# Kernel optimization log

Hardware: AMD Instinct MI355X
Metric: run time of the kernel (lower is better)

Reference implementation:

```python
import jax, jax.numpy as jnp
import numpy as np

BLOCK, HALO, HEADS, DH = 8, 4, 4, 32
EPS = 1e-5


def _convT(x, w, p):
    # torch ConvTranspose2d(stride=1, padding=p) == conv with flipped/transposed kernel, padding k-1-p
    k = w.shape[-1]
    w2 = jnp.flip(w, axis=(-2, -1)).transpose(1, 0, 2, 3)  # (Cin,Cout,k,k) -> (Cout,Cin,k,k)
    pad = k - 1 - p
    return jax.lax.conv_general_dilated(x, w2, (1, 1), ((pad, pad), (pad, pad)),
                                        dimension_numbers=('NCHW', 'OIHW', 'NCHW'))


def _bn(x, g, b, m, v):
    s = g * jax.lax.rsqrt(v + EPS)
    return x * s[None, :, None, None] + (b - m * s)[None, :, None, None]


def _rel_to_abs(x):
    # x: [b, l, 2r-1] -> [b, l, r]
    b, l, m = x.shape
    r = (m + 1) // 2
    x = jnp.concatenate([x, jnp.zeros((b, l, 1), x.dtype)], axis=2)
    flat = jnp.concatenate([x.reshape(b, l * (m + 1)), jnp.zeros((b, m - l), x.dtype)], axis=1)
    return flat.reshape(b, l + 1, m)[:, :l, -r:]


def _rel_logits_1d(q, rel_k):
    # q: [b, x, y, d]; rel_k: [2r-1, d] -> [b, x, r, y, r]
    b, x, y, d = q.shape
    r = (rel_k.shape[0] + 1) // 2
    logits = jnp.einsum('bxyd,rd->bxyr', q, rel_k)
    logits = _rel_to_abs(logits.reshape(b * x, y, -1)).reshape(b, x, y, r)
    return jnp.broadcast_to(logits[:, :, None, :, :], (b, x, r, y, r))


def _rel_pos_emb(q, rel_h, rel_w):
    # q: [bb, block*block, dh] (already scaled, per halonet-pytorch)
    bb, n, d = q.shape
    qg = q.reshape(bb, BLOCK, BLOCK, d)
    lw = _rel_logits_1d(qg, rel_w).transpose(0, 1, 3, 2, 4).reshape(bb, n, -1)  # b (x y) (i j)
    lh = _rel_logits_1d(qg.transpose(0, 2, 1, 3), rel_h).transpose(0, 3, 1, 4, 2).reshape(bb, n, -1)  # b (y x) (j i)
    return lw + lh


def _halo_attn(x, to_q, to_kv, to_out_w, to_out_b, rel_h, rel_w):
    B, C, H, W = x.shape
    b, h = BLOCK, HALO
    nh, nw = H // b, W // b
    nblk = nh * nw
    wsz = b + 2 * h
    inner = to_q.shape[1]
    scale = DH ** -0.5
    # queries: non-overlapping blocks -> [B*nblk, b*b, C]
    q_inp = x.reshape(B, C, nh, b, nw, b).transpose(0, 2, 4, 3, 5, 1).reshape(B * nblk, b * b, C)
    # keys/values: overlapping halo windows (F.unfold) -> [B*nblk, wsz*wsz, C]
    pat = jax.lax.conv_general_dilated_patches(x, (wsz, wsz), (b, b), ((h, h), (h, h)))  # [B, C*wsz*wsz, nh, nw]
    kv_inp = pat.reshape(B, C, wsz * wsz, nblk).transpose(0, 3, 2, 1).reshape(B * nblk, wsz * wsz, C)
    q = q_inp @ to_q
    k, v = jnp.split(kv_inp @ to_kv, 2, axis=-1)
    def heads(t):
        return t.reshape(t.shape[0], t.shape[1], HEADS, DH).transpose(0, 2, 1, 3).reshape(-1, t.shape[1], DH)
    q, k, v = heads(q) * scale, heads(k), heads(v)
    sim = jnp.einsum('bid,bjd->bij', q, k) + _rel_pos_emb(q, rel_h, rel_w)  # [B*nblk*HEADS, b*b, wsz*wsz]
    # mask out halo positions that fall into zero padding
    ones = jnp.ones((1, 1, H, W), x.dtype)
    mpat = jax.lax.conv_general_dilated_patches(ones, (wsz, wsz), (b, b), ((h, h), (h, h)))
    mask = mpat.reshape(wsz * wsz, nblk).T > 0  # [nblk, wsz*wsz]
    neg = -jnp.finfo(sim.dtype).max
    sim = jnp.where(mask[None, :, None, None, :],
                    sim.reshape(B, nblk, HEADS, b * b, wsz * wsz), neg)
    attn = jax.nn.softmax(sim, axis=-1).reshape(-1, b * b, wsz * wsz)
    out = jnp.einsum('bij,bjd->bid', attn, v)
    out = out.reshape(B * nblk, HEADS, b * b, DH).transpose(0, 2, 1, 3).reshape(B * nblk, b * b, inner)
    out = out @ to_out_w + to_out_b
    return out.reshape(B, nh, nw, b, b, C).transpose(0, 5, 1, 3, 2, 4).reshape(B, C, H, W)


def setup_inputs() -> dict:
    key = jax.random.key(0)
    ks = jax.random.split(key, 13)
    B, C, H, W = 2, 128, 192, 192
    inner = HEADS * DH
    rel = 2 * (BLOCK + 2 * HALO) - 1  # 31
    n = lambda k, s, sc: jax.random.normal(k, s, jnp.float32) * sc
    return {
        'x': jax.random.normal(ks[0], (B, C, H, W), jnp.float32),
        'conv1_w': n(ks[1], (C, C, 1, 1), 0.1),
        'bn1_g': jnp.ones((C,), jnp.float32), 'bn1_b': jnp.zeros((C,), jnp.float32),
        'bn1_m': n(ks[2], (C,), 0.1),
        'bn1_v': jax.random.uniform(ks[3], (C,), jnp.float32, 0.5, 1.5),
        'to_q': n(ks[4], (C, inner), 0.05), 'to_kv': n(ks[5], (C, 2 * inner), 0.05),
        'to_out_w': n(ks[6], (inner, C), 0.05), 'to_out_b': n(ks[7], (C,), 0.01),
        'rel_h': n(ks[8], (rel, DH), DH ** -0.5), 'rel_w': n(ks[9], (rel, DH), DH ** -0.5),
        'conv3_w': n(ks[10], (C, C, 3, 3), 0.05),
        'bn3_g': jnp.ones((C,), jnp.float32), 'bn3_b': jnp.zeros((C,), jnp.float32),
        'bn3_m': n(ks[11], (C,), 0.1),
        'bn3_v': jax.random.uniform(ks[12], (C,), jnp.float32, 0.5, 1.5),
    }


def reference(x, conv1_w, bn1_g, bn1_b, bn1_m, bn1_v, to_q, to_kv, to_out_w, to_out_b,
              rel_h, rel_w, conv3_w, bn3_g, bn3_b, bn3_m, bn3_v):
    # Bottleneck (stride=1, no downsample): conv1x1T -> BN -> ReLU -> HaloAttention -> ReLU
    #   -> conv3x3T -> BN -> +identity -> ReLU
    out = jax.nn.relu(_bn(_convT(x, conv1_w, 0), bn1_g, bn1_b, bn1_m, bn1_v))
    out = jax.nn.relu(_halo_attn(out, to_q, to_kv, to_out_w, to_out_b, rel_h, rel_w))
    out = _bn(_convT(out, conv3_w, 1), bn3_g, bn3_b, bn3_m, bn3_v)
    return jax.nn.relu(out + x)
```

## Files before the change

### kernel.cpp

```cpp
#include <hip/hip_runtime.h>
#include <hip/hip_bf16.h>

using bf16 = __hip_bfloat16;
typedef unsigned short u16;
typedef unsigned int   u32;
typedef __attribute__((ext_vector_type(8))) short short8;
typedef __attribute__((ext_vector_type(4))) float f32x4;

#define B_N 2
#define CCH 128
#define HH 192
#define WW 192
#define HWS (HH*WW)
#define NBLKS 576
#define EPSV 1e-5f
#define LDW 136

__device__ __forceinline__ float b2f(bf16 v){ return __bfloat162float(v); }
__device__ __forceinline__ bf16  f2b(float v){ return __float2bfloat16(v); }
__device__ __forceinline__ u32 pck(float a, float b){
    bf16 x = f2b(a), y = f2b(b);
    return (u32)*(u16*)&x | ((u32)*(u16*)&y << 16);
}

__global__ __launch_bounds__(256) void prep_w(
    const float* __restrict__ w1, const float* __restrict__ to_q,
    const float* __restrict__ to_kv, const float* __restrict__ to_ow,
    const float* __restrict__ w3, const float* __restrict__ relh,
    const float* __restrict__ relw, bf16* __restrict__ wb)
{
    int i = blockIdx.x*256 + threadIdx.x;
    float v;
    if (i < 16384){       int co=(i>>7)&127, ci=i&127;      v = w1[ci*128+co]; }
    else if (i < 32768){  int r=i-16384; int co=r>>7, ci=r&127; v = to_q[ci*128+co]*0.17677669529663687f; }
    else if (i < 49152){  int r=i-32768; int co=r>>7, ci=r&127; v = to_kv[ci*256+co]; }
    else if (i < 65536){  int r=i-49152; int co=r>>7, ci=r&127; v = to_kv[ci*256+128+co]; }
    else if (i < 81920){  int r=i-65536; int co=r>>7, ci=r&127; v = to_ow[ci*128+co]; }
    else if (i < 229376){ int r=i-81920; int tap=r>>14, co=(r>>7)&127, ci=r&127; int a=tap/3, b=tap-a*3;
                          v = w3[((size_t)(ci*128+co)*3+a)*3+b]; }
    else if (i < 230400){ int j=i-229376; v = (j < 992) ? relh[j] : 0.f; }
    else                { int j=i-230400; v = (j < 992) ? relw[j] : 0.f; }
    wb[i] = f2b(v);
}

__global__ __launch_bounds__(256) void conv1_mfma(
    const float* __restrict__ x, const bf16* __restrict__ Wp,
    bf16* __restrict__ outp,
    const float* __restrict__ bn_g, const float* __restrict__ bn_b,
    const float* __restrict__ bn_m, const float* __restrict__ bn_v)
{
    __shared__ float tF[128*68];
    __shared__ u16   sX[64*LDW];
    u16* sW = (u16*)tF;
    const int tid  = threadIdx.x;
    const int pix0 = blockIdx.x * 64;
    const int n    = pix0 / HWS;
    const int hwb  = pix0 - n*HWS;
    const int lane = tid & 63;
    const int ln = lane & 15, g = lane >> 4;
    const int cow = (tid >> 6) * 32;

    #pragma unroll
    for (int r = 0; r < 8; ++r){
        int e = tid + r*256;
        int ci = e >> 4, p4 = e & 15;
        *(float4*)&tF[ci*68 + p4*4] =
            *(const float4*)&x[(size_t)(n*CCH + ci)*HWS + hwb + p4*4];
    }
    __syncthreads();
    {
        const int pix = tid & 63, cq = tid >> 6;
        u32 pkt[16];
        #pragma unroll
        for (int c = 0; c < 16; ++c){
            int ci = cq*32 + c*2;
            pkt[c] = pck(tF[ci*68 + pix], tF[(ci+1)*68 + pix]);
        }
        u32* dst = (u32*)&sX[pix*LDW + cq*32];
        #pragma unroll
        for (int c = 0; c < 16; ++c) dst[c] = pkt[c];
    }
    __syncthreads();
    #pragma unroll
    for (int r = 0; r < 8; ++r){
        int e = tid + r*256; int row = e>>4, grp = e&15;
        *(uint4*)&sW[row*LDW + grp*8] = *(const uint4*)&Wp[row*128 + grp*8];
    }
    __syncthreads();

    f32x4 acc[4][2];
    #pragma unroll
    for (int mi=0;mi<4;mi++)
        #pragma unroll
        for (int ni=0;ni<2;ni++) acc[mi][ni] = (f32x4){0.f,0.f,0.f,0.f};
    #pragma unroll
    for (int kk = 0; kk < 4; ++kk){
        short8 fa[4], fb[2];
        #pragma unroll
        for (int mi=0;mi<4;mi++)
            fa[mi] = *(const short8*)&sX[(mi*16+ln)*LDW + kk*32 + g*8];
        #pragma unroll
        for (int ni=0;ni<2;ni++)
            fb[ni] = *(const short8*)&sW[(cow+ni*16+ln)*LDW + kk*32 + g*8];
        #pragma unroll
        for (int mi=0;mi<4;mi++)
            #pragma unroll
            for (int ni=0;ni<2;ni++)
                acc[mi][ni] = __builtin_amdgcn_mfma_f32_16x16x32_bf16(fa[mi], fb[ni], acc[mi][ni], 0, 0, 0);
    }
    float sc[2], bb[2];
    #pragma unroll
    for (int ni=0;ni<2;ni++){
        int co = cow + ni*16 + ln;
        float sg = bn_g[co]*rsqrtf(bn_v[co]+EPSV);
        sc[ni] = sg; bb[ni] = bn_b[co] - bn_m[co]*sg;
    }
    #pragma unroll
    for (int mi=0;mi<4;mi++)
        #pragma unroll
        for (int ni=0;ni<2;ni++)
            #pragma unroll
            for (int j=0;j<4;j++){
                int pix = pix0 + mi*16 + g*4 + j;
                int co  = cow + ni*16 + ln;
                float v = fmaxf(acc[mi][ni][j]*sc[ni] + bb[ni], 0.f);
                outp[(size_t)pix*CCH + co] = f2b(v);
            }
}

template<bool DO_BIAS, bool DO_RELU, bool TRANS_Y2>
__global__ __launch_bounds__(256) void gemm_mfma(
    const bf16* __restrict__ inp, const bf16* __restrict__ Wp,
    bf16* __restrict__ outp, bf16* __restrict__ outp2, int cstride, int choff,
    const float* __restrict__ bias)
{
    Wp    += (size_t)blockIdx.y * 16384;
    choff += blockIdx.y * 128;
    __shared__ u16 sW[128*LDW];
    __shared__ u16 sX[64*LDW];
    const int tid  = threadIdx.x;
    const int pix0 = blockIdx.x * 64;
    const int lane = tid & 63;
    const int ln = lane & 15, g = lane >> 4;
    const int cow = (tid >> 6) * 32;

    #pragma unroll
    for (int r = 0; r < 8; ++r){
        int e = tid + r*256; int row = e>>4, grp = e&15;
        *(uint4*)&sW[row*LDW + grp*8] = *(const uint4*)&Wp[row*128 + grp*8];
    }
    #pragma unroll
    for (int r = 0; r < 4; ++r){
        int e = tid + r*256; int row = e>>4, grp = e&15;
        *(uint4*)&sX[row*LDW + grp*8] = *(const uint4*)&inp[(size_t)(pix0+row)*CCH + grp*8];
    }
    __syncthreads();

    f32x4 acc[4][2];
    #pragma unroll
    for (int mi=0;mi<4;mi++)
        #pragma unroll
        for (int ni=0;ni<2;ni++) acc[mi][ni] = (f32x4){0.f,0.f,0.f,0.f};

    #pragma unroll
    for (int kk = 0; kk < 4; ++kk){
        short8 fa[4], fb[2];
        #pragma unroll
        for (int mi=0;mi<4;mi++)
            fa[mi] = *(const short8*)&sX[(mi*16+ln)*LDW + kk*32 + g*8];
        #pragma unroll
        for (int ni=0;ni<2;ni++)
            fb[ni] = *(const short8*)&sW[(cow+ni*16+ln)*LDW + kk*32 + g*8];
        #pragma unroll
        for (int mi=0;mi<4;mi++)
            #pragma unroll
            for (int ni=0;ni<2;ni++)
                acc[mi][ni] = __builtin_amdgcn_mfma_f32_16x16x32_bf16(fa[mi], fb[ni], acc[mi][ni], 0, 0, 0);
    }

    if (TRANS_Y2 && blockIdx.y == 2){
        __syncthreads();
        u16* tile = sX;
        #pragma unroll
        for (int mi=0;mi<4;mi++)
            #pragma unroll
            for (int ni=0;ni<2;ni++){
                int co   = cow + ni*16 + ln;
                int pixl = mi*16 + g*4;
                *(u32*)&tile[co*68 + pixl]     = pck(acc[mi][ni][0], acc[mi][ni][1]);
                *(u32*)&tile[co*68 + pixl + 2] = pck(acc[mi][ni][2], acc[mi][ni][3]);
            }
        __syncthreads();
        const int co2 = tid >> 1, hf = tid & 1;
        const int n2 = pix0 / HWS, hwb2 = pix0 - n2*HWS;
        u16* gdst = (u16*)outp2 + (size_t)(n2*CCH + co2)*HWS + hwb2 + hf*32;
        const u16* src = &tile[co2*68 + hf*32];
        #pragma unroll
        for (int k=0;k<8;k++)
            *(uint2*)&gdst[k*4] = *(const uint2*)&src[k*4];
        return;
    }

    float bb[2];
    #pragma unroll
    for (int ni=0;ni<2;ni++){
        int co = cow + ni*16 + ln;
        bb[ni] = DO_BIAS ? bias[co] : 0.f;
    }
    #pragma unroll
    for (int mi=0;mi<4;mi++)
        #pragma unroll
        for (int ni=0;ni<2;ni++)
            #pragma unroll
            for (int j=0;j<4;j++){
                int pix = pix0 + mi*16 + g*4 + j;
                int co  = cow + ni*16 + ln;
                float v = acc[mi][ni][j] + bb[ni];
                if (DO_RELU) v = fmaxf(v, 0.f);
                outp[(size_t)pix*cstride + choff + co] = f2b(v);
            }
}

__global__ __launch_bounds__(256) void conv3_mfma(
    const bf16* __restrict__ inp, const bf16* __restrict__ W3p,
    const float* __restrict__ xin, float* __restrict__ outp,
    const float* __restrict__ g3, const float* __restrict__ b3,
    const float* __restrict__ m3, const float* __restrict__ v3)
{
    __shared__ u16 sXh[66*136];
    const int tid = threadIdx.x;
    const int P0  = blockIdx.x * 64;
    const int n   = P0 / HWS;
    const int hwb = P0 - n*HWS;
    const int h = hwb / WW, wb = hwb - h*WW;
    const int lane = tid & 63, ln = lane & 15, g = lane >> 4;
    const int cow = (tid >> 6) * 32;

    f32x4 acc[2][4];
    #pragma unroll
    for (int mi=0;mi<2;mi++)
        #pragma unroll
        for (int ni=0;ni<4;ni++) acc[mi][ni] = (f32x4){0.f,0.f,0.f,0.f};

    for (int a = 0; a < 3; ++a){
        const int hs = h + 1 - a;
        if (hs < 0 || hs >= HH) continue;
        __syncthreads();
        #pragma unroll
        for (int r = 0; r < 5; ++r){
            int e = tid + r*256;
            if (e < 1056){
                int cs = e >> 4, grp = e & 15;
                int col = wb - 1 + cs;
                uint4 val = {0u,0u,0u,0u};
                if (col >= 0 && col < WW)
                    val = *(const uint4*)&inp[(size_t)(n*HWS + hs*WW + col)*CCH + grp*8];
                *(uint4*)&sXh[cs*136 + grp*8] = val;
            }
        }
        __syncthreads();
        for (int b = 0; b < 3; ++b){
            const int tap = a*3 + b;
            const bf16* Wt = W3p + tap*16384;
            #pragma unroll
            for (int kk = 0; kk < 4; ++kk){
                short8 fa[2], fb[4];
                #pragma unroll
                for (int mi=0;mi<2;mi++)
                    fa[mi] = *(const short8*)&Wt[(cow+mi*16+ln)*128 + kk*32 + g*8];
                #pragma unroll
                for (int ni=0;ni<4;ni++)
                    fb[ni] = *(const short8*)&sXh[(ni*16+ln + 2 - b)*136 + kk*32 + g*8];
                #pragma unroll
                for (int mi=0;mi<2;mi++)
                    #pragma unroll
                    for (int ni=0;ni<4;ni++)
                        acc[mi][ni] = __builtin_amdgcn_mfma_f32_16x16x32_bf16(fa[mi], fb[ni], acc[mi][ni], 0, 0, 0);
            }
        }
    }

    #pragma unroll
    for (int mi=0;mi<2;mi++)
        #pragma unroll
        for (int j=0;j<4;j++){
            int co = cow + mi*16 + g*4 + j;
            float sg = g3[co]*rsqrtf(v3[co]+EPSV);
            float bc = b3[co] - m3[co]*sg;
            #pragma unroll
            for (int ni=0;ni<4;ni++){
                int pixl = hwb + ni*16 + ln;
                size_t idx = (size_t)(n*CCH + co)*HWS + pixl;
                float v = acc[mi][ni][j]*sg + bc + xin[idx];
                outp[idx] = fmaxf(v, 0.f);
            }
        }
}

__global__ __launch_bounds__(512) void attn_kernel(
    const u16* __restrict__ QK, const u16* __restrict__ vT,
    const u16* __restrict__ relb, bf16* __restrict__ outp)
{
    __shared__ __align__(16) char smem[46848];
    u16*   sK   = (u16*)(smem);
    u16*   sP   = (u16*)(smem);
    u16*   sVT  = (u16*)(smem + 20480);
    float* tT   = (float*)(smem + 37376);
    float* wredM= (float*)(smem + 45824);
    float* wredS= (float*)(smem + 46336);

    const int tid  = threadIdx.x;
    const int bid0 = blockIdx.x;
    const int bid  = (bid0 & 7) * 576 + (bid0 >> 3);
    const int head = bid & 3;
    const int t    = bid >> 2;
    const int n    = t / NBLKS;
    const int blk  = t - n*NBLKS;
    const int bi = blk / 24, bj = blk - bi*24;
    const int row0 = bi*8 - 4, col0 = bj*8 - 4;
    const int ch0 = head*32;
    const int wv = tid >> 6, lane = tid & 63, ln = lane & 15, g = lane >> 4;
    const int nt = wv & 3, mh = wv >> 2;

    uint2 vreg[4];
    #pragma unroll
    for (int r = 0; r < 4; ++r){
        int e = tid + r*512;
        int d   = e >> 6;
        int rem = e & 63;
        int iw  = rem >> 2;
        int jc  = (rem & 3) * 4;
        int rr  = row0 + iw, cc0 = col0 + jc;
        uint2 vv = {0u,0u};
        if (rr >= 0 && rr < HH && cc0 >= 0 && cc0 < 189)
            vv = *(const uint2*)&vT[(size_t)(n*CCH + ch0 + d)*HWS + rr*WW + cc0];
        vreg[r] = vv;
    }

    #pragma unroll
    for (int r = 0; r < 2; ++r){
        int e = tid + r*512;
        int wp = e >> 2, q4 = e & 3;
        int rr = row0 + (wp>>4), cc2 = col0 + (wp&15);
        uint4 kk4 = {0u,0u,0u,0u};
        if (rr>=0 && rr<HH && cc2>=0 && cc2<WW){
            size_t P = (size_t)n*HWS + rr*WW + cc2;
            kk4 = *(const uint4*)&QK[P*256 + 128 + ch0 + q4*8];
        }
        *(uint4*)&sK[wp*40 + q4*8] = kk4;
    }

    const int qc = nt*16 + ln;
    size_t Pq = (size_t)n*HWS + (bi*8 + (qc>>3))*WW + bj*8 + (qc&7);
    const short8 qfrag = *(const short8*)&QK[Pq*256 + ch0 + g*8];
    __syncthreads();

    f32x4 accs[8];
    #pragma unroll
    for (int i=0;i<8;i++){
        short8 fk = *(const short8*)&sK[((mh*8+i)*16+ln)*40 + g*8];
        accs[i] = __builtin_amdgcn_mfma_f32_16x16x32_bf16(fk, qfrag, (f32x4){0.f,0.f,0.f,0.f}, 0, 0, 0);
    }

    {
        const u16* relX = relb + (mh ? 1024 : 0);
        #pragma unroll
        for (int ntr=0; ntr<2; ++ntr){
            short8 fr = *(const short8*)&relX[(ntr*16+ln)*32 + g*8];
            f32x4 L = __builtin_amdgcn_mfma_f32_16x16x32_bf16(qfrag, fr, (f32x4){0.f,0.f,0.f,0.f}, 0, 0, 0);
            #pragma unroll
            for (int r2=0;r2<4;r2++){
                int q  = nt*16 + g*4 + r2;
                int rr = ntr*16 + ln;
                int bq = mh ? (q&7) : (q>>3);
                int iw = rr - 15 + bq;
                if (iw >= 0 && iw < 16) tT[mh*1056 + iw*66 + q] = L[r2];
            }
        }
    }
    __syncthreads();

    float tw[4];
    bool cok[4];
    #pragma unroll
    for (int r2=0;r2<4;r2++){
        tw[r2] = tT[1056 + (g*4+r2)*66 + qc];
        int cc2 = col0 + g*4 + r2;
        cok[r2] = (cc2 >= 0 && cc2 < WW);
    }
    float mx = -3.4e38f;
    #pragma unroll
    for (int i=0;i<8;i++){
        int mt = mh*8 + i;
        int rr = row0 + mt;
        bool rok = (rr >= 0 && rr < HH);
        float th = tT[mt*66 + qc];
        #pragma unroll
        for (int r2=0;r2<4;r2++){
            float s = (rok && cok[r2]) ? (accs[i][r2] + th + tw[r2]) : -3.0e38f;
            accs[i][r2] = s;
            mx = fmaxf(mx, s);
        }
    }
    mx = fmaxf(mx, __shfl_xor(mx, 16));
    mx = fmaxf(mx, __shfl_xor(mx, 32));
    if (g == 0) wredM[mh*64 + qc] = mx;
    __syncthreads();

    #pragma unroll
    for (int r = 0; r < 4; ++r){
        int e = tid + r*512;
        int d   = e >> 6;
        int rem = e & 63;
        int iw  = rem >> 2;
        int jc  = (rem & 3) * 4;
        *(uint2*)&sVT[d*264 + iw*16 + jc] = vreg[r];
    }
    mx = fmaxf(wredM[qc], wredM[64 + qc]);

    float sm = 0.f;
    #pragma unroll
    for (int i=0;i<8;i++){
        #pragma unroll
        for (int r2=0;r2<4;r2++){
            float p = __expf(accs[i][r2] - mx);
            accs[i][r2] = p;
            sm += p;
        }
    }
    sm += __shfl_xor(sm, 16);
    sm += __shfl_xor(sm, 32);
    if (g == 0) wredS[mh*64 + qc] = sm;
    if (mh == 0){
        #pragma unroll
        for (int i=0;i<8;i++){
            u32* dst = (u32*)&sP[qc*136 + i*16 + g*4];
            dst[0] = pck(accs[i][0], accs[i][1]);
            dst[1] = pck(accs[i][2], accs[i][3]);
        }
    }
    __syncthreads();

    const int dt = wv & 1, qt = wv >> 1;
    f32x4 acco = (f32x4){0.f,0.f,0.f,0.f};
    #pragma unroll
    for (int ks=0; ks<4; ++ks){
        short8 fa = *(const short8*)&sVT[(dt*16+ln)*264 + ks*32 + g*8];
        short8 fb = *(const short8*)&sP [(qt*16+ln)*136 + ks*32 + g*8];
        acco = __builtin_amdgcn_mfma_f32_16x16x32_bf16(fa, fb, acco, 0, 0, 0);
    }
    __syncthreads();
    if (mh == 1){
        #pragma unroll
        for (int i=0;i<8;i++){
            u32* dst = (u32*)&sP[qc*136 + i*16 + g*4];
            dst[0] = pck(accs[i][0], accs[i][1]);
            dst[1] = pck(accs[i][2], accs[i][3]);
        }
    }
    __syncthreads();

    #pragma unroll
    for (int ks=0; ks<4; ++ks){
        short8 fa = *(const short8*)&sVT[(dt*16+ln)*264 + 128 + ks*32 + g*8];
        short8 fb = *(const short8*)&sP [(qt*16+ln)*136 + ks*32 + g*8];
        acco = __builtin_amdgcn_mfma_f32_16x16x32_bf16(fa, fb, acco, 0, 0, 0);
    }
    {
        const int q = qt*16 + ln;
        const float inv = 1.f / (wredS[q] + wredS[64 + q]);
        size_t P = (size_t)n*HWS + (bi*8 + (q>>3))*WW + bj*8 + (q&7);
        uint2 ov;
        ov.x = pck(acco[0]*inv, acco[1]*inv);
        ov.y = pck(acco[2]*inv, acco[3]*inv);
        *(uint2*)&outp[P*CCH + ch0 + dt*16 + g*4] = ov;
    }
}

extern "C" void kernel_launch(void* const* d_in, const int* in_sizes, int n_in,
                              void* d_out, int out_size, void* d_ws, size_t ws_size,
                              hipStream_t stream)
{
    (void)in_sizes; (void)n_in; (void)out_size; (void)ws_size;
    const float* x      = (const float*)d_in[0];
    const float* w1     = (const float*)d_in[1];
    const float* bn1_g  = (const float*)d_in[2];
    const float* bn1_b  = (const float*)d_in[3];
    const float* bn1_m  = (const float*)d_in[4];
    const float* bn1_v  = (const float*)d_in[5];
    const float* to_q   = (const float*)d_in[6];
    const float* to_kv  = (const float*)d_in[7];
    const float* to_ow  = (const float*)d_in[8];
    const float* to_ob  = (const float*)d_in[9];
    const float* rel_h  = (const float*)d_in[10];
    const float* rel_w  = (const float*)d_in[11];
    const float* w3     = (const float*)d_in[12];
    const float* bn3_g  = (const float*)d_in[13];
    const float* bn3_b  = (const float*)d_in[14];
    const float* bn3_m  = (const float*)d_in[15];
    const float* bn3_v  = (const float*)d_in[16];

    char* ws   = (char*)d_ws;
    bf16* out1 = (bf16*)(ws + 0);
    bf16* qk   = (bf16*)(ws + 18874368);
    bf16* vT   = (bf16*)(ws + 75497472);
    bf16* wb   = (bf16*)(ws + 94371840);
    bf16* W3p  = wb + 81920;
    u16*  relb = (u16*)(wb + 229376);
    bf16* attnout = (bf16*)d_out;
    bf16* out2    = out1;

    prep_w<<<904, 256, 0, stream>>>(w1, to_q, to_kv, to_ow, w3, rel_h, rel_w, wb);

    conv1_mfma<<<1152, 256, 0, stream>>>(x, wb, out1, bn1_g, bn1_b, bn1_m, bn1_v);
    gemm_mfma<false,false,true><<<dim3(1152,3), 256, 0, stream>>>(
        out1, wb + 16384, qk, vT, 256, 0, nullptr);

    attn_kernel<<<4608, 512, 0, stream>>>((const u16*)qk, (const u16*)vT,
                                          relb, attnout);

    gemm_mfma<true,true,false><<<dim3(1152,1), 256, 0, stream>>>(
        attnout, wb + 65536, out2, nullptr, 128, 0, to_ob);

    conv3_mfma<<<1152, 256, 0, stream>>>(out2, W3p, x, (float*)d_out,
                                         bn3_g, bn3_b, bn3_m, bn3_v);
}
```

Before: 176.5 us.

## Split conv3 output channels across two blocks and stage weights in LDS with prefetch

The conv3 kernel now launches twice as many blocks, each computing 64 output channels instead of 128, so each wave holds one 16-channel tile and fewer accumulators. Per-tap weights are staged into shared memory, and the next tap's weights are prefetched into registers while the current tap's MFMAs run, replacing direct global loads of weight fragments. The aims are better occupancy and less global weight traffic. In exchange, each input halo row is loaded twice (once per channel half) and more barriers are added.

```diff
diff --git a/kernel.cpp b/kernel.cpp
--- a/kernel.cpp
+++ b/kernel.cpp
@@ -227,28 +227,31 @@
     const float* __restrict__ g3, const float* __restrict__ b3,
     const float* __restrict__ m3, const float* __restrict__ v3)
 {
+    __shared__ u16 sW[64*136];
     __shared__ u16 sXh[66*136];
-    const int tid = threadIdx.x;
-    const int P0  = blockIdx.x * 64;
-    const int n   = P0 / HWS;
-    const int hwb = P0 - n*HWS;
+    const int tid  = threadIdx.x;
+    const int half = blockIdx.x & 1;
+    const int P0   = (blockIdx.x >> 1) * 64;
+    const int co0  = half * 64;
+    const int n    = P0 / HWS;
+    const int hwb  = P0 - n*HWS;
     const int h = hwb / WW, wb = hwb - h*WW;
     const int lane = tid & 63, ln = lane & 15, g = lane >> 4;
-    const int cow = (tid >> 6) * 32;
-
-    f32x4 acc[2][4];
-    #pragma unroll
-    for (int mi=0;mi<2;mi++)
-        #pragma unroll
-        for (int ni=0;ni<4;ni++) acc[mi][ni] = (f32x4){0.f,0.f,0.f,0.f};
+    const int w = tid >> 6;
+
+    const int se  = tid;
+    f32x4 acc[4];
+    #pragma unroll
+    for (int ni=0;ni<4;ni++) acc[ni] = (f32x4){0.f,0.f,0.f,0.f};
 
     for (int a = 0; a < 3; ++a){
         const int hs = h + 1 - a;
         if (hs < 0 || hs >= HH) continue;
+        const int tap0 = a*3;
         __syncthreads();
         #pragma unroll
         for (int r = 0; r < 5; ++r){
-            int e = tid + r*256;
+            int e = se + r*256;
             if (e < 1056){
                 int cs = e >> 4, grp = e & 15;
                 int col = wb - 1 + cs;
@@ -258,43 +261,82 @@
                 *(uint4*)&sXh[cs*136 + grp*8] = val;
             }
         }
-        __syncthreads();
-        for (int b = 0; b < 3; ++b){
-            const int tap = a*3 + b;
-            const bf16* Wt = W3p + tap*16384;
-            #pragma unroll
-            for (int kk = 0; kk < 4; ++kk){
-                short8 fa[2], fb[4];
-                #pragma unroll
-                for (int mi=0;mi<2;mi++)
-                    fa[mi] = *(const short8*)&Wt[(cow+mi*16+ln)*128 + kk*32 + g*8];
-                #pragma unroll
-                for (int ni=0;ni<4;ni++)
-                    fb[ni] = *(const short8*)&sXh[(ni*16+ln + 2 - b)*136 + kk*32 + g*8];
-                #pragma unroll
-                for (int mi=0;mi<2;mi++)
-                    #pragma unroll
-                    for (int ni=0;ni<4;ni++)
-                        acc[mi][ni] = __builtin_amdgcn_mfma_f32_16x16x32_bf16(fa[mi], fb[ni], acc[mi][ni], 0, 0, 0);
-            }
-        }
-    }
-
-    #pragma unroll
-    for (int mi=0;mi<2;mi++)
-        #pragma unroll
-        for (int j=0;j<4;j++){
-            int co = cow + mi*16 + g*4 + j;
-            float sg = g3[co]*rsqrtf(v3[co]+EPSV);
-            float bc = b3[co] - m3[co]*sg;
-            #pragma unroll
-            for (int ni=0;ni<4;ni++){
-                int pixl = hwb + ni*16 + ln;
-                size_t idx = (size_t)(n*CCH + co)*HWS + pixl;
-                float v = acc[mi][ni][j]*sg + bc + xin[idx];
-                outp[idx] = fmaxf(v, 0.f);
-            }
-        }
+        #pragma unroll
+        for (int r = 0; r < 4; ++r){
+            int e = se + r*256; int row = e>>4, grp = e&15;
+            *(uint4*)&sW[row*136 + grp*8] =
+                *(const uint4*)&W3p[(size_t)tap0*16384 + (co0+row)*128 + grp*8];
+        }
+        __syncthreads();
+
+        uint4 wA[4];
+        #pragma unroll
+        for (int r = 0; r < 4; ++r){
+            int e = se + r*256; int row = e>>4, grp = e&15;
+            wA[r] = *(const uint4*)&W3p[(size_t)(tap0+1)*16384 + (co0+row)*128 + grp*8];
+        }
+        #pragma unroll
+        for (int kk=0;kk<4;++kk){
+            short8 fa = *(const short8*)&sW[(w*16+ln)*136 + kk*32 + g*8];
+            #pragma unroll
+            for (int ni=0;ni<4;++ni){
+                short8 fb = *(const short8*)&sXh[(ni*16+ln+2)*136 + kk*32 + g*8];
+                acc[ni] = __builtin_amdgcn_mfma_f32_16x16x32_bf16(fa, fb, acc[ni], 0, 0, 0);
+            }
+        }
+        __syncthreads();
+        #pragma unroll
+        for (int r = 0; r < 4; ++r){
+            int e = se + r*256; int row = e>>4, grp = e&15;
+            *(uint4*)&sW[row*136 + grp*8] = wA[r];
+        }
+        uint4 wB[4];
+        #pragma unroll
+        for (int r = 0; r < 4; ++r){
+            int e = se + r*256; int row = e>>4, grp = e&15;
+            wB[r] = *(const uint4*)&W3p[(size_t)(tap0+2)*16384 + (co0+row)*128 + grp*8];
+        }
+        __syncthreads();
+        #pragma unroll
+        for (int kk=0;kk<4;++kk){
+            short8 fa = *(const short8*)&sW[(w*16+ln)*136 + kk*32 + g*8];
+            #pragma unroll
+            for (int ni=0;ni<4;++ni){
+                short8 fb = *(const short8*)&sXh[(ni*16+ln+1)*136 + kk*32 + g*8];
+                acc[ni] = __builtin_amdgcn_mfma_f32_16x16x32_bf16(fa, fb, acc[ni], 0, 0, 0);
+            }
+        }
+        __syncthreads();
+        #pragma unroll
+        for (int r = 0; r < 4; ++r){
+            int e = se + r*256; int row = e>>4, grp = e&15;
+            *(uint4*)&sW[row*136 + grp*8] = wB[r];
+        }
+        __syncthreads();
+        #pragma unroll
+        for (int kk=0;kk<4;++kk){
+            short8 fa = *(const short8*)&sW[(w*16+ln)*136 + kk*32 + g*8];
+            #pragma unroll
+            for (int ni=0;ni<4;++ni){
+                short8 fb = *(const short8*)&sXh[(ni*16+ln)*136 + kk*32 + g*8];
+                acc[ni] = __builtin_amdgcn_mfma_f32_16x16x32_bf16(fa, fb, acc[ni], 0, 0, 0);
+            }
+        }
+    }
+
+    #pragma unroll
+    for (int j=0;j<4;++j){
+        int co = co0 + w*16 + g*4 + j;
+        float sg = g3[co]*rsqrtf(v3[co]+EPSV);
+        float bc = b3[co] - m3[co]*sg;
+        #pragma unroll
+        for (int ni=0;ni<4;++ni){
+            int pixl = hwb + ni*16 + ln;
+            size_t idx = (size_t)(n*CCH + co)*HWS + pixl;
+            float v = acc[ni][j]*sg + bc + xin[idx];
+            outp[idx] = fmaxf(v, 0.f);
+        }
+    }
 }
 
 __global__ __launch_bounds__(512) void attn_kernel(
@@ -522,6 +564,6 @@
     gemm_mfma<true,true,false><<<dim3(1152,1), 256, 0, stream>>>(
         attnout, wb + 65536, out2, nullptr, 128, 0, to_ob);
 
-    conv3_mfma<<<1152, 256, 0, stream>>>(out2, W3p, x, (float*)d_out,
+    conv3_mfma<<<2304, 256, 0, stream>>>(out2, W3p, x, (float*)d_out,
                                          bn3_g, bn3_b, bn3_m, bn3_v);
 }
```

Result: slower. 196.1 us (+11.1%).
